# Kernel tuning notes

Measured on AMD Instinct MI355X. Metric: run time of the kernel, lower is better.

Reference implementation:

```python
import jax, jax.numpy as jnp
import numpy as np

B, S, D, N, HD, M = 2, 2048, 1024, 16, 64, 4096  # batch, seq, d_model, heads, head_dim, d_mlp


def setup_inputs() -> dict:
    key = jax.random.key(0)
    ks = jax.random.split(key, 8)
    sd = 1.0 / np.sqrt(D)
    return {
        "x": jax.random.normal(ks[0], (B, S, D), dtype=jnp.float32),
        "W_qkv": jax.random.normal(ks[1], (N, D, 3 * HD), dtype=jnp.float32) * sd,
        "W_out": jax.random.normal(ks[2], (N, HD, D), dtype=jnp.float32) * sd,
        "ln1_w": jnp.ones((D,), jnp.float32),
        "ln1_b": jnp.zeros((D,), jnp.float32),
        "ln2_w": jnp.ones((D,), jnp.float32),
        "ln2_b": jnp.zeros((D,), jnp.float32),
        "W1": jax.random.normal(ks[3], (D, M), dtype=jnp.float32) * sd,
        "b1": jnp.zeros((M,), jnp.float32),
        "W2": jax.random.normal(ks[4], (M, D), dtype=jnp.float32) / np.sqrt(M),
        "b2": jnp.zeros((D,), jnp.float32),
    }


def _layernorm(x, w, b, eps=1e-4):
    mu = jnp.mean(x, axis=-1, keepdims=True)
    var = jnp.var(x, axis=-1, keepdims=True, ddof=1)  # torch unbiased var
    return w * (x - mu) / jnp.sqrt(var + eps) + b


def _attention(x, W_qkv, W_out):
    b, s, d = x.shape
    qkv = jnp.einsum('bsd,ndh->bnsh', x, W_qkv)  # [b,n,s,3*hd]
    q, k, v = jnp.split(qkv, 3, axis=-1)
    hd = q.shape[-1]
    attn = jnp.einsum('bnqh,bnkh->bnqk', q, k) / np.sqrt(hd)
    mask = -1e10 * (1.0 - jnp.tril(jnp.ones((s, s), jnp.float32)))
    attn = jax.nn.softmax(attn + mask, axis=-1)
    out = jnp.einsum('bnqk,bnkh->bnqh', attn, v)  # [b,n,s,hd]
    # faithful to torch: raw memory reinterpretation (b,n,s,hd) -> (b, n*hd, s)
    out = out.reshape(b, -1, s)
    # faithful to torch: d is a shared free index -> W_out summed over (n,h)
    out = jnp.einsum('bds,nhd->bsd', out, W_out)
    return out


def _mlp(x, W1, b1, W2, b2):
    h = jax.nn.gelu(x @ W1 + b1, approximate=False)
    return h @ W2 + b2


def reference(x, W_qkv, W_out, ln1_w, ln1_b, ln2_w, ln2_b, W1, b1, W2, b2):
    x = x + _attention(_layernorm(x, ln1_w, ln1_b), W_qkv, W_out)
    x = x + _mlp(_layernorm(x, ln2_w, ln2_b), W1, b1, W2, b2)
    return x
```

## Files before the change

kernel.cpp:

```cpp
#include <hip/hip_runtime.h>

typedef unsigned short ushort_t;
typedef __attribute__((ext_vector_type(8))) short short8;
typedef __attribute__((ext_vector_type(4))) float floatx4;
typedef __attribute__((ext_vector_type(4))) unsigned short ushort4v;

#define B_ 2
#define S_ 2048
#define D_ 1024
#define NH_ 16
#define HD_ 64
#define M_ 4096

#define KSCALE 0.18033688011112042f

__device__ __forceinline__ ushort_t f2bf(float f) {
    unsigned u = __builtin_bit_cast(unsigned, f);
    return (ushort_t)((u + 0x7FFFu + ((u >> 16) & 1u)) >> 16);
}

__device__ __forceinline__ void gload_lds16(const ushort_t* g, ushort_t* l) {
    __builtin_amdgcn_global_load_lds(
        (const __attribute__((address_space(1))) unsigned int*)(g),
        (__attribute__((address_space(3))) unsigned int*)(l), 16, 0, 0);
}

__device__ __forceinline__ ushort_t to_bf_elem(float f) { return f2bf(f); }
__device__ __forceinline__ ushort_t to_bf_elem(ushort_t u) { return u; }

template <typename T>
__global__ __launch_bounds__(256) void transpose_to_bf16(
    const T* __restrict__ src, ushort_t* __restrict__ dst,
    int R, int C, long sbatch, long dbatch, int srs, int drs) {
    __shared__ ushort_t tile[32][33];
    src += (size_t)blockIdx.z * sbatch;
    dst += (size_t)blockIdx.z * dbatch;
    int c = blockIdx.x * 32 + threadIdx.x;
    #pragma unroll
    for (int i = 0; i < 4; ++i) {
        int r = blockIdx.y * 32 + threadIdx.y + i * 8;
        if (r < R && c < C) tile[threadIdx.y + i * 8][threadIdx.x] = to_bf_elem(src[(size_t)r * srs + c]);
    }
    __syncthreads();
    int rr = blockIdx.y * 32 + threadIdx.x;
    #pragma unroll
    for (int i = 0; i < 4; ++i) {
        int cc = blockIdx.x * 32 + threadIdx.y + i * 8;
        if (cc < C && rr < R) dst[(size_t)cc * drs + rr] = tile[threadIdx.x][threadIdx.y + i * 8];
    }
}

__global__ __launch_bounds__(256) void wsum_kernel(const float* __restrict__ W_out,
                                                   float* __restrict__ wsum) {
    int col = blockIdx.x * 32 + (threadIdx.x & 31);
    int rg = threadIdx.x >> 5;
    float s = 0.f;
    for (int r = rg; r < NH_ * HD_; r += 8) s += W_out[(size_t)r * D_ + col];
    __shared__ float part[256];
    part[threadIdx.x] = s;
    __syncthreads();
    if (threadIdx.x < 32) {
        float t = 0.f;
        #pragma unroll
        for (int g = 0; g < 8; ++g) t += part[g * 32 + threadIdx.x];
        wsum[blockIdx.x * 32 + threadIdx.x] = t;
    }
}

__global__ __launch_bounds__(256) void ln1_kernel(const float* __restrict__ x,
                                                  const float* __restrict__ w,
                                                  const float* __restrict__ b,
                                                  ushort_t* __restrict__ out) {
    int row = blockIdx.x, tid = threadIdx.x;
    float v[4], s = 0.f, ss = 0.f;
    #pragma unroll
    for (int i = 0; i < 4; ++i) {
        v[i] = x[(size_t)row * D_ + tid + i * 256];
        s += v[i]; ss += v[i] * v[i];
    }
    #pragma unroll
    for (int off = 32; off >= 1; off >>= 1) { s += __shfl_xor(s, off); ss += __shfl_xor(ss, off); }
    __shared__ float red[8];
    if ((tid & 63) == 0) { red[(tid >> 6) * 2] = s; red[(tid >> 6) * 2 + 1] = ss; }
    __syncthreads();
    s = red[0] + red[2] + red[4] + red[6];
    ss = red[1] + red[3] + red[5] + red[7];
    float mu = s * (1.f / D_);
    float var = (ss - (float)D_ * mu * mu) * (1.f / (D_ - 1));
    float rstd = rsqrtf(var + 1e-4f);
    #pragma unroll
    for (int i = 0; i < 4; ++i) {
        int d = tid + i * 256;
        out[(size_t)row * D_ + d] = f2bf((v[i] - mu) * rstd * w[d] + b[d]);
    }
}

__global__ __launch_bounds__(256) void gather_resid(
    const float* __restrict__ x, const float* __restrict__ attn,
    const float* __restrict__ wsum, float* __restrict__ x1) {
    __shared__ float tile[128][65];
    const int tid = threadIdx.x;
    const int dchunk = blockIdx.x;
    const int stile = blockIdx.y;
    const int b = stile >> 5, shi = stile & 31;
    const int h = tid & 63;
    const int wv = tid >> 6;
    #pragma unroll
    for (int r = 0; r < 32; ++r) {
        int dloc = r * 4 + wv;
        int d = dchunk * 128 + dloc;
        int q = ((d & 63) << 5) + shi;
        tile[dloc][h] = attn[((size_t)(b * NH_ + (d >> 6)) * S_ + q) * HD_ + h];
    }
    __syncthreads();
    const int row0 = b * S_ + shi * 64;
    #pragma unroll
    for (int r = 0; r < 32; ++r) {
        int sr = r * 2 + (tid >> 7);
        int dcol = tid & 127;
        int d = dchunk * 128 + dcol;
        size_t idx = (size_t)(row0 + sr) * D_ + d;
        x1[idx] = x[idx] + wsum[d] * tile[dcol][sr];
    }
}

template <int EPI>
__global__ __launch_bounds__(256) void gemm_bt(
    const ushort_t* __restrict__ A, const ushort_t* __restrict__ BT,
    int M, int N, int K, int ld, const float* __restrict__ bias,
    const float* __restrict__ resid, void* __restrict__ outp) {
    __shared__ __align__(16) ushort_t As[128 * 64];
    __shared__ __align__(16) ushort_t Bs[128 * 64];
    const int tid = threadIdx.x;
    const int lane = tid & 63, wave = tid >> 6;
    const int ln15 = lane & 15, qd = lane >> 4;
    const int wm = wave >> 1, wn = wave & 1;
    const int bm = blockIdx.y, bn = blockIdx.x;
    const int lr = lane >> 3;
    const int sw = (lane & 7) ^ lr;
    if (EPI == 3) {
        A += (size_t)blockIdx.z * K;
        BT += (size_t)blockIdx.z * K;
    }

    floatx4 acc[4][4];
    #pragma unroll
    for (int i = 0; i < 4; ++i)
        #pragma unroll
        for (int j = 0; j < 4; ++j) acc[i][j] = (floatx4){0.f, 0.f, 0.f, 0.f};

    for (int k0 = 0; k0 < K; k0 += 64) {
        __syncthreads();
        #pragma unroll
        for (int l = 0; l < 4; ++l) {
            int r0 = (l * 4 + wave) * 8;
            gload_lds16(A + (size_t)(bm * 128 + r0 + lr) * ld + k0 + sw * 8, &As[r0 * 64]);
            gload_lds16(BT + (size_t)(bn * 128 + r0 + lr) * ld + k0 + sw * 8, &Bs[r0 * 64]);
        }
        __syncthreads();
        #pragma unroll
        for (int ks = 0; ks < 2; ++ks) {
            short8 a[4], b[4];
            #pragma unroll
            for (int mt = 0; mt < 4; ++mt) {
                int row = wm * 64 + mt * 16 + ln15;
                a[mt] = *(const short8*)&As[row * 64 + (((ks * 4 + qd) ^ (row & 7)) << 3)];
            }
            #pragma unroll
            for (int nt = 0; nt < 4; ++nt) {
                int row = wn * 64 + nt * 16 + ln15;
                b[nt] = *(const short8*)&Bs[row * 64 + (((ks * 4 + qd) ^ (row & 7)) << 3)];
            }
            #pragma unroll
            for (int mt = 0; mt < 4; ++mt)
                #pragma unroll
                for (int nt = 0; nt < 4; ++nt)
                    acc[mt][nt] = __builtin_amdgcn_mfma_f32_16x16x32_bf16(a[mt], b[nt], acc[mt][nt], 0, 0, 0);
        }
    }

    const int row0 = bm * 128 + wm * 64, col0 = bn * 128 + wn * 64;
    #pragma unroll
    for (int mt = 0; mt < 4; ++mt)
        #pragma unroll
        for (int nt = 0; nt < 4; ++nt)
            #pragma unroll
            for (int r = 0; r < 4; ++r) {
                int row = row0 + mt * 16 + qd * 4 + r;
                int col = col0 + nt * 16 + ln15;
                float v = acc[mt][nt][r];
                if (EPI == 0) {
                    int bb = row >> 11, sidx = row & 2047;
                    unsigned uc = (unsigned)col;
                    unsigned hn = uc / 192u;
                    unsigned j = uc - hn * 192u;
                    if (j >= 64u && j < 128u) v *= KSCALE;
                    ((ushort_t*)outp)[(((size_t)bb * NH_ + hn) * S_ + sidx) * 192 + j] = f2bf(v);
                } else if (EPI == 1) {
                    v += bias[col];
                    float g = 0.5f * v * (1.0f + erff(v * 0.70710678118654752f));
                    ((ushort_t*)outp)[(size_t)row * N + col] = f2bf(g);
                } else if (EPI == 2) {
                    v += bias[col] + resid[(size_t)row * N + col];
                    ((float*)outp)[(size_t)row * N + col] = v;
                } else {
                    float* po = (float*)outp + (size_t)blockIdx.z * M * N;
                    po[(size_t)row * N + col] = v;
                }
            }
}

__global__ __launch_bounds__(256) void mlp2_reduce(const float* __restrict__ part,
                                                   const float* __restrict__ b2,
                                                   const float* __restrict__ x1,
                                                   float* __restrict__ out) {
    const size_t NTOT = (size_t)B_ * S_ * D_;
    size_t i = ((size_t)blockIdx.x * 256 + threadIdx.x) * 4;
    floatx4 s = *(const floatx4*)(part + i);
    s += *(const floatx4*)(part + NTOT + i);
    s += *(const floatx4*)(part + 2 * NTOT + i);
    s += *(const floatx4*)(part + 3 * NTOT + i);
    int col = (int)(i & (D_ - 1));
    s += *(const floatx4*)(b2 + col);
    s += *(const floatx4*)(x1 + i);
    *(floatx4*)(out + i) = s;
}

__global__ __launch_bounds__(256) void attn_kernel(const ushort_t* __restrict__ qkv,
                                                   const ushort_t* __restrict__ vT,
                                                   float* __restrict__ attn_out) {
    __shared__ __align__(16) ushort_t Ks[128 * 64];
    __shared__ __align__(16) ushort_t Vs[64 * 128];
    __shared__ __align__(16) ushort_t Ps[4][16 * 72];
    const int tid = threadIdx.x, lane = tid & 63, w = tid >> 6;
    const int ln15 = lane & 15, qd = lane >> 4;
    const int qt = (int)gridDim.x - 1 - (int)blockIdx.x;
    const int bh = blockIdx.z * NH_ + blockIdx.y;
    const int qb = qt * 64 + w * 16;
    const size_t qbase = (size_t)bh * S_ * 192;
    const size_t vtbase = (size_t)bh * HD_ * S_;
    ushort_t* myP = (ushort_t*)Ps[w];

    const ushort_t* qrow = qkv + qbase + (size_t)(qb + ln15) * 192;
    short8 bq[2];
    bq[0] = *(const short8*)(qrow + qd * 8);
    bq[1] = *(const short8*)(qrow + 32 + qd * 8);

    float lcur = 0.f;
    floatx4 oacc[4];
    #pragma unroll
    for (int mt = 0; mt < 4; ++mt) oacc[mt] = (floatx4){0.f, 0.f, 0.f, 0.f};

    const int ntiles = qt + 1;
    for (int kt2 = 0; kt2 < ntiles; kt2 += 2) {
        __syncthreads();
        #pragma unroll
        for (int i = 0; i < 4; ++i) {
            int gb = (i * 4 + w) * 64;
            int g = gb + lane;
            int krow = g >> 3;
            int kcg = (g & 7) ^ (krow & 7);
            int key = kt2 * 64 + krow; if (key > S_ - 1) key = S_ - 1;
            gload_lds16(qkv + qbase + (size_t)key * 192 + 64 + kcg * 8, &Ks[gb * 8]);
            int vrow = g >> 4;
            int vcg = (g & 15) ^ (vrow & 15);
            int vkey = kt2 * 64 + vcg * 8; if (vkey > S_ - 8) vkey = S_ - 8;
            gload_lds16(vT + vtbase + (size_t)vrow * S_ + vkey, &Vs[gb * 8]);
        }
        __syncthreads();

        int nk = ntiles - kt2; if (nk > 2) nk = 2;
        for (int kh = 0; kh < nk; ++kh) {
            floatx4 sacc[4];
            #pragma unroll
            for (int mt = 0; mt < 4; ++mt) sacc[mt] = (floatx4){0.f, 0.f, 0.f, 0.f};
            #pragma unroll
            for (int ks = 0; ks < 2; ++ks)
                #pragma unroll
                for (int mt = 0; mt < 4; ++mt) {
                    int row = kh * 64 + mt * 16 + ln15;
                    short8 ak = *(const short8*)&Ks[row * 64 + (((ks * 4 + qd) ^ (row & 7)) << 3)];
                    sacc[mt] = __builtin_amdgcn_mfma_f32_16x16x32_bf16(ak, bq[ks], sacc[mt], 0, 0, 0);
                }
            if (kt2 + kh == qt) {
                int q = qb + ln15;
                #pragma unroll
                for (int mt = 0; mt < 4; ++mt)
                    #pragma unroll
                    for (int r = 0; r < 4; ++r)
                        if (qt * 64 + mt * 16 + qd * 4 + r > q) sacc[mt][r] = -1e30f;
            }
            float rsum = 0.f;
            #pragma unroll
            for (int mt = 0; mt < 4; ++mt) {
                ushort4v pk;
                #pragma unroll
                for (int r = 0; r < 4; ++r) {
                    float p = exp2f(sacc[mt][r]);
                    rsum += p;
                    pk[r] = (ushort_t)(__builtin_bit_cast(unsigned, p) >> 16);
                }
                *(ushort4v*)&myP[ln15 * 72 + mt * 16 + qd * 4] = pk;
            }
            rsum += __shfl_xor(rsum, 16);
            rsum += __shfl_xor(rsum, 32);
            lcur += rsum;
            #pragma unroll
            for (int g2 = 0; g2 < 2; ++g2) {
                short8 bp = *(const short8*)&myP[ln15 * 72 + g2 * 32 + qd * 8];
                #pragma unroll
                for (int mt = 0; mt < 4; ++mt) {
                    int row = mt * 16 + ln15;
                    short8 av = *(const short8*)&Vs[row * 128 + (((kh * 8 + g2 * 4 + qd) ^ (row & 15)) << 3)];
                    oacc[mt] = __builtin_amdgcn_mfma_f32_16x16x32_bf16(av, bp, oacc[mt], 0, 0, 0);
                }
            }
        }
    }
    float inv = 1.f / lcur;
    int q = qb + ln15;
    #pragma unroll
    for (int mt = 0; mt < 4; ++mt) {
        floatx4 o = oacc[mt] * inv;
        *(floatx4*)&attn_out[((size_t)bh * S_ + q) * HD_ + mt * 16 + qd * 4] = o;
    }
}

extern "C" void kernel_launch(void* const* d_in, const int* in_sizes, int n_in,
                              void* d_out, int out_size, void* d_ws, size_t ws_size,
                              hipStream_t stream) {
    const float* x = (const float*)d_in[0];
    const float* W_qkv = (const float*)d_in[1];
    const float* W_out = (const float*)d_in[2];
    const float* ln1_w = (const float*)d_in[3];
    const float* ln1_b = (const float*)d_in[4];
    const float* ln2_w = (const float*)d_in[5];
    const float* ln2_b = (const float*)d_in[6];
    const float* W1 = (const float*)d_in[7];
    const float* b1 = (const float*)d_in[8];
    const float* W2 = (const float*)d_in[9];
    const float* b2 = (const float*)d_in[10];

    char* ws = (char*)d_ws;
    const size_t MB = 1024 * 1024;
    ushort_t* ln1_out = (ushort_t*)(ws + 0 * MB);
    ushort_t* WqkvT   = (ushort_t*)(ws + 8 * MB);
    ushort_t* qkv     = (ushort_t*)(ws + 14 * MB);
    ushort_t* vT      = (ushort_t*)(ws + 38 * MB);
    float*    attn_o  = (float*)(ws + 46 * MB);
    float*    partials = (float*)(ws + 0 * MB);
    float*    x1      = (float*)(ws + 64 * MB);
    ushort_t* ln2_out = (ushort_t*)(ws + 80 * MB);
    ushort_t* W1T     = (ushort_t*)(ws + 88 * MB);
    ushort_t* hbuf    = (ushort_t*)(ws + 96 * MB);
    ushort_t* W2T     = (ushort_t*)(ws + 128 * MB);
    float*    wsum    = (float*)(ws + 136 * MB);

    dim3 tb(32, 8);
    transpose_to_bf16<float><<<dim3(192 / 32, D_ / 32, NH_), tb, 0, stream>>>(
        W_qkv, WqkvT, D_, 192, (long)D_ * 192, (long)192 * D_, 192, D_);
    transpose_to_bf16<float><<<dim3(M_ / 32, D_ / 32, 1), tb, 0, stream>>>(
        W1, W1T, D_, M_, 0, 0, M_, D_);
    transpose_to_bf16<float><<<dim3(D_ / 32, M_ / 32, 1), tb, 0, stream>>>(
        W2, W2T, M_, D_, 0, 0, D_, M_);
    wsum_kernel<<<dim3(D_ / 32), 256, 0, stream>>>(W_out, wsum);
    ln1_kernel<<<dim3(B_ * S_), 256, 0, stream>>>(x, ln1_w, ln1_b, ln1_out);
    gemm_bt<0><<<dim3(3072 / 128, (B_ * S_) / 128), 256, 0, stream>>>(
        ln1_out, WqkvT, B_ * S_, 3072, D_, D_, nullptr, nullptr, qkv);
    transpose_to_bf16<ushort_t><<<dim3(HD_ / 32, S_ / 32, B_ * NH_), tb, 0, stream>>>(
        qkv + 128, vT, S_, HD_, (long)S_ * 192, (long)HD_ * S_, 192, S_);
    attn_kernel<<<dim3(S_ / 64, NH_, B_), 256, 0, stream>>>(qkv, vT, attn_o);
    gather_resid<<<dim3(8, 64), 256, 0, stream>>>(x, attn_o, wsum, x1);
    ln1_kernel<<<dim3(B_ * S_), 256, 0, stream>>>(x1, ln2_w, ln2_b, ln2_out);
    gemm_bt<1><<<dim3(M_ / 128, (B_ * S_) / 128), 256, 0, stream>>>(
        ln2_out, W1T, B_ * S_, M_, D_, D_, b1, nullptr, hbuf);
    gemm_bt<3><<<dim3(D_ / 128, (B_ * S_) / 128, 4), 256, 0, stream>>>(
        hbuf, W2T, B_ * S_, D_, M_ / 4, M_, nullptr, nullptr, partials);
    mlp2_reduce<<<dim3((B_ * S_ * D_) / 1024), 256, 0, stream>>>(partials, b2, x1, (float*)d_out);
}
```

Before: 445.7 us.

## Fuse weight prep kernels, write V transposed from QKV GEMM, use tanh-GELU, interleave attention

```diff
diff --git a/kernel.cpp b/kernel.cpp
--- a/kernel.cpp
+++ b/kernel.cpp
@@ -25,45 +25,59 @@
         (__attribute__((address_space(3))) unsigned int*)(l), 16, 0, 0);
 }
 
-__device__ __forceinline__ ushort_t to_bf_elem(float f) { return f2bf(f); }
-__device__ __forceinline__ ushort_t to_bf_elem(ushort_t u) { return u; }
-
-template <typename T>
-__global__ __launch_bounds__(256) void transpose_to_bf16(
-    const T* __restrict__ src, ushort_t* __restrict__ dst,
-    int R, int C, long sbatch, long dbatch, int srs, int drs) {
+__device__ __forceinline__ void transpose_body(
+    const float* __restrict__ src, ushort_t* __restrict__ dst,
+    int R, int C, int srs, int drs, int bx, int by, int tx, int ty,
+    ushort_t (*tile)[33]) {
+    int c = bx * 32 + tx;
+    #pragma unroll
+    for (int i = 0; i < 4; ++i) {
+        int r = by * 32 + ty + i * 8;
+        if (r < R && c < C) tile[ty + i * 8][tx] = f2bf(src[(size_t)r * srs + c]);
+    }
+    __syncthreads();
+    int rr = by * 32 + tx;
+    #pragma unroll
+    for (int i = 0; i < 4; ++i) {
+        int cc = bx * 32 + ty + i * 8;
+        if (cc < C && rr < R) dst[(size_t)cc * drs + rr] = tile[tx][ty + i * 8];
+    }
+}
+
+__global__ __launch_bounds__(256) void prep_kernel(
+    const float* __restrict__ W_qkv, const float* __restrict__ W1,
+    const float* __restrict__ W2, const float* __restrict__ W_out,
+    ushort_t* __restrict__ WqkvT, ushort_t* __restrict__ W1T,
+    ushort_t* __restrict__ W2T, float* __restrict__ wsum) {
     __shared__ ushort_t tile[32][33];
-    src += (size_t)blockIdx.z * sbatch;
-    dst += (size_t)blockIdx.z * dbatch;
-    int c = blockIdx.x * 32 + threadIdx.x;
-    #pragma unroll
-    for (int i = 0; i < 4; ++i) {
-        int r = blockIdx.y * 32 + threadIdx.y + i * 8;
-        if (r < R && c < C) tile[threadIdx.y + i * 8][threadIdx.x] = to_bf_elem(src[(size_t)r * srs + c]);
-    }
-    __syncthreads();
-    int rr = blockIdx.y * 32 + threadIdx.x;
-    #pragma unroll
-    for (int i = 0; i < 4; ++i) {
-        int cc = blockIdx.x * 32 + threadIdx.y + i * 8;
-        if (cc < C && rr < R) dst[(size_t)cc * drs + rr] = tile[threadIdx.x][threadIdx.y + i * 8];
-    }
-}
-
-__global__ __launch_bounds__(256) void wsum_kernel(const float* __restrict__ W_out,
-                                                   float* __restrict__ wsum) {
-    int col = blockIdx.x * 32 + (threadIdx.x & 31);
-    int rg = threadIdx.x >> 5;
-    float s = 0.f;
-    for (int r = rg; r < NH_ * HD_; r += 8) s += W_out[(size_t)r * D_ + col];
-    __shared__ float part[256];
-    part[threadIdx.x] = s;
-    __syncthreads();
-    if (threadIdx.x < 32) {
-        float t = 0.f;
-        #pragma unroll
-        for (int g = 0; g < 8; ++g) t += part[g * 32 + threadIdx.x];
-        wsum[blockIdx.x * 32 + threadIdx.x] = t;
+    const int bid = blockIdx.x;
+    const int tx = threadIdx.x & 31, ty = threadIdx.x >> 5;
+    if (bid < 3072) {
+        int bz = bid / 192, rem = bid % 192;
+        int bx = rem % 6, by = rem / 6;
+        transpose_body(W_qkv + (size_t)bz * D_ * 192, WqkvT + (size_t)bz * 192 * D_,
+                       D_, 192, 192, D_, bx, by, tx, ty, tile);
+    } else if (bid < 3072 + 4096) {
+        int r = bid - 3072;
+        transpose_body(W1, W1T, D_, M_, M_, D_, r % 128, r / 128, tx, ty, tile);
+    } else if (bid < 3072 + 8192) {
+        int r = bid - 7168;
+        transpose_body(W2, W2T, M_, D_, D_, M_, r % 32, r / 32, tx, ty, tile);
+    } else {
+        int cb = bid - 11264;
+        float* part = (float*)tile;
+        int col = cb * 32 + tx;
+        int rg = threadIdx.x >> 5;
+        float s = 0.f;
+        for (int r = rg; r < NH_ * HD_; r += 8) s += W_out[(size_t)r * D_ + col];
+        part[threadIdx.x] = s;
+        __syncthreads();
+        if (threadIdx.x < 32) {
+            float t = 0.f;
+            #pragma unroll
+            for (int g = 0; g < 8; ++g) t += part[g * 32 + threadIdx.x];
+            wsum[cb * 32 + threadIdx.x] = t;
+        }
     }
 }
 
@@ -128,7 +142,7 @@
 __global__ __launch_bounds__(256) void gemm_bt(
     const ushort_t* __restrict__ A, const ushort_t* __restrict__ BT,
     int M, int N, int K, int ld, const float* __restrict__ bias,
-    const float* __restrict__ resid, void* __restrict__ outp) {
+    const float* __restrict__ resid, void* __restrict__ outp, void* __restrict__ outp2) {
     __shared__ __align__(16) ushort_t As[128 * 64];
     __shared__ __align__(16) ushort_t Bs[128 * 64];
     const int tid = threadIdx.x;
@@ -183,31 +197,50 @@
     #pragma unroll
     for (int mt = 0; mt < 4; ++mt)
         #pragma unroll
-        for (int nt = 0; nt < 4; ++nt)
-            #pragma unroll
-            for (int r = 0; r < 4; ++r) {
-                int row = row0 + mt * 16 + qd * 4 + r;
+        for (int nt = 0; nt < 4; ++nt) {
+            if (EPI == 0) {
                 int col = col0 + nt * 16 + ln15;
-                float v = acc[mt][nt][r];
-                if (EPI == 0) {
-                    int bb = row >> 11, sidx = row & 2047;
-                    unsigned uc = (unsigned)col;
-                    unsigned hn = uc / 192u;
-                    unsigned j = uc - hn * 192u;
-                    if (j >= 64u && j < 128u) v *= KSCALE;
-                    ((ushort_t*)outp)[(((size_t)bb * NH_ + hn) * S_ + sidx) * 192 + j] = f2bf(v);
-                } else if (EPI == 1) {
-                    v += bias[col];
-                    float g = 0.5f * v * (1.0f + erff(v * 0.70710678118654752f));
-                    ((ushort_t*)outp)[(size_t)row * N + col] = f2bf(g);
-                } else if (EPI == 2) {
-                    v += bias[col] + resid[(size_t)row * N + col];
-                    ((float*)outp)[(size_t)row * N + col] = v;
+                unsigned uc = (unsigned)col;
+                unsigned hn = uc / 192u;
+                unsigned j = uc - hn * 192u;
+                int rowb = row0 + mt * 16 + qd * 4;
+                int bb = rowb >> 11, sidx = rowb & 2047;
+                if (j < 128u) {
+                    #pragma unroll
+                    for (int r = 0; r < 4; ++r) {
+                        float v = acc[mt][nt][r];
+                        if (j >= 64u) v *= KSCALE;
+                        ((ushort_t*)outp)[(((size_t)bb * NH_ + hn) * S_ + sidx + r) * 192 + j] = f2bf(v);
+                    }
                 } else {
-                    float* po = (float*)outp + (size_t)blockIdx.z * M * N;
-                    po[(size_t)row * N + col] = v;
+                    ushort4v pk;
+                    #pragma unroll
+                    for (int r = 0; r < 4; ++r) pk[r] = f2bf(acc[mt][nt][r]);
+                    *(ushort4v*)&((ushort_t*)outp2)[((size_t)(bb * NH_ + hn) * HD_ + (j - 128u)) * S_ + sidx] = pk;
                 }
-            }
+            } else {
+                #pragma unroll
+                for (int r = 0; r < 4; ++r) {
+                    int row = row0 + mt * 16 + qd * 4 + r;
+                    int col = col0 + nt * 16 + ln15;
+                    float v = acc[mt][nt][r];
+                    if (EPI == 1) {
+                        v += bias[col];
+                        float u = v * (0.7978845608f + 0.0356774081f * v * v);
+                        float e = exp2f(fminf(u * 2.88539008f, 80.f));
+                        float rc = __builtin_amdgcn_rcpf(e + 1.f);
+                        float g = v * (1.f - rc);
+                        ((ushort_t*)outp)[(size_t)row * N + col] = f2bf(g);
+                    } else if (EPI == 2) {
+                        v += bias[col] + resid[(size_t)row * N + col];
+                        ((float*)outp)[(size_t)row * N + col] = v;
+                    } else {
+                        float* po = (float*)outp + (size_t)blockIdx.z * M * N;
+                        po[(size_t)row * N + col] = v;
+                    }
+                }
+            }
+        }
 }
 
 __global__ __launch_bounds__(256) void mlp2_reduce(const float* __restrict__ part,
@@ -251,6 +284,54 @@
     #pragma unroll
     for (int mt = 0; mt < 4; ++mt) oacc[mt] = (floatx4){0.f, 0.f, 0.f, 0.f};
 
+    auto qk_half = [&](int kh, floatx4* s) {
+        #pragma unroll
+        for (int mt = 0; mt < 4; ++mt) s[mt] = (floatx4){0.f, 0.f, 0.f, 0.f};
+        #pragma unroll
+        for (int ks = 0; ks < 2; ++ks)
+            #pragma unroll
+            for (int mt = 0; mt < 4; ++mt) {
+                int row = kh * 64 + mt * 16 + ln15;
+                short8 ak = *(const short8*)&Ks[row * 64 + (((ks * 4 + qd) ^ (row & 7)) << 3)];
+                s[mt] = __builtin_amdgcn_mfma_f32_16x16x32_bf16(ak, bq[ks], s[mt], 0, 0, 0);
+            }
+    };
+    auto softmax_pv = [&](floatx4* s, int kh, bool mask) {
+        if (mask) {
+            int q = qb + ln15;
+            #pragma unroll
+            for (int mt = 0; mt < 4; ++mt)
+                #pragma unroll
+                for (int r = 0; r < 4; ++r)
+                    if (qt * 64 + mt * 16 + qd * 4 + r > q) s[mt][r] = -1e30f;
+        }
+        float rsum = 0.f;
+        #pragma unroll
+        for (int mt = 0; mt < 4; ++mt) {
+            ushort4v pk;
+            #pragma unroll
+            for (int r = 0; r < 4; ++r) {
+                float p = exp2f(s[mt][r]);
+                rsum += p;
+                pk[r] = (ushort_t)(__builtin_bit_cast(unsigned, p) >> 16);
+            }
+            *(ushort4v*)&myP[ln15 * 72 + mt * 16 + qd * 4] = pk;
+        }
+        rsum += __shfl_xor(rsum, 16);
+        rsum += __shfl_xor(rsum, 32);
+        lcur += rsum;
+        #pragma unroll
+        for (int g2 = 0; g2 < 2; ++g2) {
+            short8 bp = *(const short8*)&myP[ln15 * 72 + g2 * 32 + qd * 8];
+            #pragma unroll
+            for (int mt = 0; mt < 4; ++mt) {
+                int row = mt * 16 + ln15;
+                short8 av = *(const short8*)&Vs[row * 128 + (((kh * 8 + g2 * 4 + qd) ^ (row & 15)) << 3)];
+                oacc[mt] = __builtin_amdgcn_mfma_f32_16x16x32_bf16(av, bp, oacc[mt], 0, 0, 0);
+            }
+        }
+    };
+
     const int ntiles = qt + 1;
     for (int kt2 = 0; kt2 < ntiles; kt2 += 2) {
         __syncthreads();
@@ -269,52 +350,16 @@
         }
         __syncthreads();
 
-        int nk = ntiles - kt2; if (nk > 2) nk = 2;
-        for (int kh = 0; kh < nk; ++kh) {
-            floatx4 sacc[4];
-            #pragma unroll
-            for (int mt = 0; mt < 4; ++mt) sacc[mt] = (floatx4){0.f, 0.f, 0.f, 0.f};
-            #pragma unroll
-            for (int ks = 0; ks < 2; ++ks)
-                #pragma unroll
-                for (int mt = 0; mt < 4; ++mt) {
-                    int row = kh * 64 + mt * 16 + ln15;
-                    short8 ak = *(const short8*)&Ks[row * 64 + (((ks * 4 + qd) ^ (row & 7)) << 3)];
-                    sacc[mt] = __builtin_amdgcn_mfma_f32_16x16x32_bf16(ak, bq[ks], sacc[mt], 0, 0, 0);
-                }
-            if (kt2 + kh == qt) {
-                int q = qb + ln15;
-                #pragma unroll
-                for (int mt = 0; mt < 4; ++mt)
-                    #pragma unroll
-                    for (int r = 0; r < 4; ++r)
-                        if (qt * 64 + mt * 16 + qd * 4 + r > q) sacc[mt][r] = -1e30f;
-            }
-            float rsum = 0.f;
-            #pragma unroll
-            for (int mt = 0; mt < 4; ++mt) {
-                ushort4v pk;
-                #pragma unroll
-                for (int r = 0; r < 4; ++r) {
-                    float p = exp2f(sacc[mt][r]);
-                    rsum += p;
-                    pk[r] = (ushort_t)(__builtin_bit_cast(unsigned, p) >> 16);
-                }
-                *(ushort4v*)&myP[ln15 * 72 + mt * 16 + qd * 4] = pk;
-            }
-            rsum += __shfl_xor(rsum, 16);
-            rsum += __shfl_xor(rsum, 32);
-            lcur += rsum;
-            #pragma unroll
-            for (int g2 = 0; g2 < 2; ++g2) {
-                short8 bp = *(const short8*)&myP[ln15 * 72 + g2 * 32 + qd * 8];
-                #pragma unroll
-                for (int mt = 0; mt < 4; ++mt) {
-                    int row = mt * 16 + ln15;
-                    short8 av = *(const short8*)&Vs[row * 128 + (((kh * 8 + g2 * 4 + qd) ^ (row & 15)) << 3)];
-                    oacc[mt] = __builtin_amdgcn_mfma_f32_16x16x32_bf16(av, bp, oacc[mt], 0, 0, 0);
-                }
-            }
+        if (kt2 + 1 < ntiles) {
+            floatx4 s0[4], s1[4];
+            qk_half(0, s0);
+            qk_half(1, s1);
+            softmax_pv(s0, 0, false);
+            softmax_pv(s1, 1, kt2 + 1 == qt);
+        } else {
+            floatx4 s0[4];
+            qk_half(0, s0);
+            softmax_pv(s0, 0, kt2 == qt);
         }
     }
     float inv = 1.f / lcur;
@@ -356,25 +401,16 @@
     ushort_t* W2T     = (ushort_t*)(ws + 128 * MB);
     float*    wsum    = (float*)(ws + 136 * MB);
 
-    dim3 tb(32, 8);
-    transpose_to_bf16<float><<<dim3(192 / 32, D_ / 32, NH_), tb, 0, stream>>>(
-        W_qkv, WqkvT, D_, 192, (long)D_ * 192, (long)192 * D_, 192, D_);
-    transpose_to_bf16<float><<<dim3(M_ / 32, D_ / 32, 1), tb, 0, stream>>>(
-        W1, W1T, D_, M_, 0, 0, M_, D_);
-    transpose_to_bf16<float><<<dim3(D_ / 32, M_ / 32, 1), tb, 0, stream>>>(
-        W2, W2T, M_, D_, 0, 0, D_, M_);
-    wsum_kernel<<<dim3(D_ / 32), 256, 0, stream>>>(W_out, wsum);
+    prep_kernel<<<dim3(11296), 256, 0, stream>>>(W_qkv, W1, W2, W_out, WqkvT, W1T, W2T, wsum);
     ln1_kernel<<<dim3(B_ * S_), 256, 0, stream>>>(x, ln1_w, ln1_b, ln1_out);
     gemm_bt<0><<<dim3(3072 / 128, (B_ * S_) / 128), 256, 0, stream>>>(
-        ln1_out, WqkvT, B_ * S_, 3072, D_, D_, nullptr, nullptr, qkv);
-    transpose_to_bf16<ushort_t><<<dim3(HD_ / 32, S_ / 32, B_ * NH_), tb, 0, stream>>>(
-        qkv + 128, vT, S_, HD_, (long)S_ * 192, (long)HD_ * S_, 192, S_);
+        ln1_out, WqkvT, B_ * S_, 3072, D_, D_, nullptr, nullptr, qkv, vT);
     attn_kernel<<<dim3(S_ / 64, NH_, B_), 256, 0, stream>>>(qkv, vT, attn_o);
     gather_resid<<<dim3(8, 64), 256, 0, stream>>>(x, attn_o, wsum, x1);
     ln1_kernel<<<dim3(B_ * S_), 256, 0, stream>>>(x1, ln2_w, ln2_b, ln2_out);
     gemm_bt<1><<<dim3(M_ / 128, (B_ * S_) / 128), 256, 0, stream>>>(
-        ln2_out, W1T, B_ * S_, M_, D_, D_, b1, nullptr, hbuf);
+        ln2_out, W1T, B_ * S_, M_, D_, D_, b1, nullptr, hbuf, nullptr);
     gemm_bt<3><<<dim3(D_ / 128, (B_ * S_) / 128, 4), 256, 0, stream>>>(
-        hbuf, W2T, B_ * S_, D_, M_ / 4, M_, nullptr, nullptr, partials);
+        hbuf, W2T, B_ * S_, D_, M_ / 4, M_, nullptr, nullptr, partials, nullptr);
     mlp2_reduce<<<dim3((B_ * S_ * D_) / 1024), 256, 0, stream>>>(partials, b2, x1, (float*)d_out);
 }
```

Measured after the change: 432.5 us. 3.0% less time.
